# Performance work log

Measured on AMD Instinct MI355X. Metric: run time of the kernel, lower is better.

## Reference

```python
import jax, jax.numpy as jnp
import numpy as np

B, LC, LQ, D = 16, 2048, 1024, 512


def setup_inputs() -> dict:
    key = jax.random.key(0)
    k1, k2, k3 = jax.random.split(key, 3)
    context = jax.random.normal(k1, (B, LC, D), dtype=jnp.float32)
    query = jax.random.normal(k2, (LQ, D), dtype=jnp.float32)
    # nn.Linear(3*D, 1, bias=False).weight  -> [1, 3D]
    w = jax.random.normal(k3, (1, 3 * D), dtype=jnp.float32) * (1.0 / np.sqrt(3 * D))
    return {"context": context, "query": query, "w": w}


def reference(context, query, w):
    # context: [B, Lc, D], query: [Lq, D], w: [1, 3D]
    d = context.shape[-1]
    wc, wq, wm = w[0, :d], w[0, d:2 * d], w[0, 2 * d:]
    # S[b,i,j] = <context[b,i], wc> + <query[j], wq> + <context[b,i]*wm, query[j]>
    # (algebraic collapse of Linear(cat(c, q, c*q)) -- identical math, no 4D tensor)
    S = ((context @ wc)[:, :, None]
         + (query @ wq)[None, None, :]
         + jnp.einsum('bid,jd->bij', context * wm, query))  # [B, Lc, Lq]
    # softmax over context dim (dim=1), then permute -> A[b,j,i]
    A = jnp.transpose(jax.nn.softmax(S, axis=1), (0, 2, 1))  # [B, Lq, Lc]
    # query mask: sign(|sum_d query|), same for every batch element
    qmask = jnp.sign(jnp.abs(jnp.sum(query, axis=-1)))  # [Lq]
    A = A * qmask[None, :, None]
    # attd[b,j,i,d] = A[b,j,i] * context[b,i,d]
    # G_att[b,i,d] = context[b,i,d] * sum_j A[b,j,i]
    colsum = jnp.sum(A, axis=1)  # [B, Lc]
    G_att = context * colsum[:, :, None]  # [B, Lc, D]
    # H[b,j,d] = sum_i A[b,j,i] * context[b,i,d]
    H = jnp.einsum('bji,bid->bjd', A, context)  # [B, Lq, D]
    G = jnp.concatenate((context, G_att), axis=2)  # [B, Lc, 2D]
    return (G, H)
```

## Files before the change

### kernel.cpp

```cpp
#include <hip/hip_runtime.h>
#include <stdint.h>

#define BB 16
#define LC 2048
#define LQ 1024
#define DD 512

typedef _Float16 f16x8 __attribute__((ext_vector_type(8)));
typedef _Float16 f16x4 __attribute__((ext_vector_type(4)));
typedef float f32x4 __attribute__((ext_vector_type(4)));

#define MFMA16 __builtin_amdgcn_mfma_f32_16x16x32_f16

__global__ void zero_k(float* __restrict__ p, int n) {
    int i = blockIdx.x * blockDim.x + threadIdx.x;
    if (i < n) p[i] = 0.0f;
}

__global__ __launch_bounds__(256) void prep_ctx(
    const float* __restrict__ ctx, const float* __restrict__ w,
    _Float16* __restrict__ cm, _Float16* __restrict__ ct, float* __restrict__ cb)
{
    __shared__ _Float16 sm[64][68];
    const int b = blockIdx.z;
    const int i0 = blockIdx.y * 64;
    const int d0 = blockIdx.x * 64;
    const int t = threadIdx.x;
    const int tx = t & 15, ty = t >> 4;
    const float* wc = w;
    const float* wm = w + 2 * DD;
    const float4 wc4 = *(const float4*)(wc + d0 + tx * 4);
    const float4 wm4 = *(const float4*)(wm + d0 + tx * 4);
    for (int k = 0; k < 4; ++k) {
        const int r = ty + 16 * k;
        const int ig = i0 + r;
        const float4 v = *(const float4*)(ctx + ((size_t)(b * LC + ig)) * DD + d0 + tx * 4);
        f16x4 cmv = { (_Float16)(v.x * wm4.x), (_Float16)(v.y * wm4.y),
                      (_Float16)(v.z * wm4.z), (_Float16)(v.w * wm4.w) };
        *(f16x4*)(cm + ((size_t)(b * LC + ig)) * DD + d0 + tx * 4) = cmv;
        sm[tx * 4 + 0][r] = (_Float16)v.x;
        sm[tx * 4 + 1][r] = (_Float16)v.y;
        sm[tx * 4 + 2][r] = (_Float16)v.z;
        sm[tx * 4 + 3][r] = (_Float16)v.w;
        float p = v.x * wc4.x + v.y * wc4.y + v.z * wc4.z + v.w * wc4.w;
        p += __shfl_xor(p, 1); p += __shfl_xor(p, 2);
        p += __shfl_xor(p, 4); p += __shfl_xor(p, 8);
        if (tx == 0) atomicAdd(&cb[b * LC + ig], p);
    }
    __syncthreads();
    for (int k = 0; k < 4; ++k) {
        const int dd = ty + 16 * k;
        f16x4 o = *(const f16x4*)(&sm[dd][tx * 4]);
        *(f16x4*)(ct + ((size_t)(b * DD + d0 + dd)) * LC + i0 + tx * 4) = o;
    }
}

__global__ __launch_bounds__(128) void prep_q(
    const float* __restrict__ q, const float* __restrict__ w,
    _Float16* __restrict__ qh, float* __restrict__ qb, float* __restrict__ qmask)
{
    const int j = blockIdx.x;
    const int t = threadIdx.x;
    const float* wq = w + DD;
    const float4 v = *(const float4*)(q + (size_t)j * DD + t * 4);
    const float4 wq4 = *(const float4*)(wq + t * 4);
    f16x4 qv = { (_Float16)v.x, (_Float16)v.y, (_Float16)v.z, (_Float16)v.w };
    *(f16x4*)(qh + (size_t)j * DD + t * 4) = qv;
    float dq = v.x * wq4.x + v.y * wq4.y + v.z * wq4.z + v.w * wq4.w;
    float sq = v.x + v.y + v.z + v.w;
    for (int m = 1; m < 64; m <<= 1) { dq += __shfl_xor(dq, m); sq += __shfl_xor(sq, m); }
    __shared__ float sd[2], ss[2];
    if ((t & 63) == 0) { sd[t >> 6] = dq; ss[t >> 6] = sq; }
    __syncthreads();
    if (t == 0) {
        qb[j] = sd[0] + sd[1];
        float s = ss[0] + ss[1];
        qmask[j] = (s != 0.0f) ? 1.0f : 0.0f;
    }
}

__global__ __launch_bounds__(256) void gemm1(
    const _Float16* __restrict__ qh, const _Float16* __restrict__ cm,
    const float* __restrict__ cb, const float* __restrict__ qb,
    _Float16* __restrict__ E, float* __restrict__ lsum)
{
    __shared__ __align__(16) _Float16 smA[128 * 40];
    __shared__ __align__(16) _Float16 smB[128 * 40];
    const int b = blockIdx.z;
    const int m0 = blockIdx.x * 128;
    const int n0 = blockIdx.y * 128;
    const int t = threadIdx.x;
    const int lane = t & 63;
    const int wid = t >> 6;
    const int wvm = wid >> 1, wvn = wid & 1;
    const int li = lane & 15, lg = lane >> 4;
    f32x4 acc[4][4] = {};
    const int sr = t >> 1;
    const int sc = (t & 1) * 16;
    const _Float16* Ap = qh + (size_t)(m0 + sr) * DD + sc;
    const _Float16* Bp = cm + ((size_t)(b * LC + n0 + sr)) * DD + sc;
    _Float16* sAp = smA + sr * 40 + sc;
    _Float16* sBp = smB + sr * 40 + sc;
    for (int ks = 0; ks < DD; ks += 32) {
        uint4 a0 = *(const uint4*)(Ap + ks);
        uint4 a1 = *(const uint4*)(Ap + ks + 8);
        uint4 b0 = *(const uint4*)(Bp + ks);
        uint4 b1 = *(const uint4*)(Bp + ks + 8);
        __syncthreads();
        *(uint4*)(sAp) = a0;
        *(uint4*)(sAp + 8) = a1;
        *(uint4*)(sBp) = b0;
        *(uint4*)(sBp + 8) = b1;
        __syncthreads();
        const int ch = lg * 8;
        f16x8 af[4], bf[4];
        #pragma unroll
        for (int mt = 0; mt < 4; ++mt)
            af[mt] = *(const f16x8*)(smA + (wvm * 64 + mt * 16 + li) * 40 + ch);
        #pragma unroll
        for (int nt = 0; nt < 4; ++nt)
            bf[nt] = *(const f16x8*)(smB + (wvn * 64 + nt * 16 + li) * 40 + ch);
        #pragma unroll
        for (int mt = 0; mt < 4; ++mt)
            #pragma unroll
            for (int nt = 0; nt < 4; ++nt)
                acc[mt][nt] = MFMA16(af[mt], bf[nt], acc[mt][nt], 0, 0, 0);
    }
    __syncthreads();
    float* rs = (float*)smA;
    if (t < 128) rs[t] = 0.0f;
    __syncthreads();
    float cbv[4];
    #pragma unroll
    for (int nt = 0; nt < 4; ++nt) cbv[nt] = cb[b * LC + n0 + wvn * 64 + nt * 16 + li];
    #pragma unroll
    for (int mt = 0; mt < 4; ++mt) {
        #pragma unroll
        for (int r = 0; r < 4; ++r) {
            const int jl = wvm * 64 + mt * 16 + lg * 4 + r;
            const int j = m0 + jl;
            const float qbv = qb[j];
            _Float16* Erow = E + ((size_t)(b * LQ + j)) * LC + n0 + wvn * 64;
            float rsv = 0.0f;
            #pragma unroll
            for (int nt = 0; nt < 4; ++nt) {
                float e = __expf(acc[mt][nt][r] + cbv[nt] + qbv);
                rsv += e;
                Erow[nt * 16 + li] = (_Float16)e;
            }
            rsv += __shfl_xor(rsv, 1); rsv += __shfl_xor(rsv, 2);
            rsv += __shfl_xor(rsv, 4); rsv += __shfl_xor(rsv, 8);
            if (li == 0) atomicAdd(&rs[jl], rsv);
        }
    }
    __syncthreads();
    if (t < 128) atomicAdd(&lsum[b * LQ + m0 + t], rs[t]);
}

__global__ __launch_bounds__(256) void gemm2(
    const _Float16* __restrict__ E, const _Float16* __restrict__ ct,
    const float* __restrict__ lsum, const float* __restrict__ qmask,
    float* __restrict__ H)
{
    __shared__ __align__(16) _Float16 smA[128 * 40];
    __shared__ __align__(16) _Float16 smB[128 * 40];
    const int b = blockIdx.z;
    const int m0 = blockIdx.x * 128;
    const int n0 = blockIdx.y * 128;
    const int t = threadIdx.x;
    const int lane = t & 63;
    const int wid = t >> 6;
    const int wvm = wid >> 1, wvn = wid & 1;
    const int li = lane & 15, lg = lane >> 4;
    f32x4 acc[4][4] = {};
    const int sr = t >> 1;
    const int sc = (t & 1) * 16;
    const _Float16* Ap = E + ((size_t)(b * LQ + m0 + sr)) * LC + sc;
    const _Float16* Bp = ct + ((size_t)(b * DD + n0 + sr)) * LC + sc;
    _Float16* sAp = smA + sr * 40 + sc;
    _Float16* sBp = smB + sr * 40 + sc;
    for (int ks = 0; ks < LC; ks += 32) {
        uint4 a0 = *(const uint4*)(Ap + ks);
        uint4 a1 = *(const uint4*)(Ap + ks + 8);
        uint4 b0 = *(const uint4*)(Bp + ks);
        uint4 b1 = *(const uint4*)(Bp + ks + 8);
        __syncthreads();
        *(uint4*)(sAp) = a0;
        *(uint4*)(sAp + 8) = a1;
        *(uint4*)(sBp) = b0;
        *(uint4*)(sBp + 8) = b1;
        __syncthreads();
        const int ch = lg * 8;
        f16x8 af[4], bf[4];
        #pragma unroll
        for (int mt = 0; mt < 4; ++mt)
            af[mt] = *(const f16x8*)(smA + (wvm * 64 + mt * 16 + li) * 40 + ch);
        #pragma unroll
        for (int nt = 0; nt < 4; ++nt)
            bf[nt] = *(const f16x8*)(smB + (wvn * 64 + nt * 16 + li) * 40 + ch);
        #pragma unroll
        for (int mt = 0; mt < 4; ++mt)
            #pragma unroll
            for (int nt = 0; nt < 4; ++nt)
                acc[mt][nt] = MFMA16(af[mt], bf[nt], acc[mt][nt], 0, 0, 0);
    }
    #pragma unroll
    for (int mt = 0; mt < 4; ++mt) {
        #pragma unroll
        for (int r = 0; r < 4; ++r) {
            const int j = m0 + wvm * 64 + mt * 16 + lg * 4 + r;
            const float s = qmask[j] / lsum[b * LQ + j];
            float* Hrow = H + ((size_t)(b * LQ + j)) * DD + n0 + wvn * 64;
            #pragma unroll
            for (int nt = 0; nt < 4; ++nt)
                Hrow[nt * 16 + li] = acc[mt][nt][r] * s;
        }
    }
}

__global__ __launch_bounds__(256) void colsum_k(
    const _Float16* __restrict__ E, const float* __restrict__ lsum,
    const float* __restrict__ qmask, float* __restrict__ cs)
{
    __shared__ float ssm[256];
    const int b = blockIdx.z;
    const int i = blockIdx.x * 256 + threadIdx.x;
    const int j0 = blockIdx.y * 256;
    const int jj = j0 + threadIdx.x;
    ssm[threadIdx.x] = qmask[jj] / lsum[b * LQ + jj];
    __syncthreads();
    const _Float16* Eb = E + ((size_t)(b * LQ + j0)) * LC + i;
    float acc = 0.0f;
    #pragma unroll 4
    for (int j = 0; j < 256; ++j)
        acc += (float)Eb[(size_t)j * LC] * ssm[j];
    atomicAdd(&cs[b * LC + i], acc);
}

__global__ __launch_bounds__(128) void gwrite(
    const float* __restrict__ ctx, const float* __restrict__ cs, float* __restrict__ G)
{
    const int b = blockIdx.y, i = blockIdx.x, t = threadIdx.x;
    const float c = cs[b * LC + i];
    const size_t ro = (size_t)(b * LC + i);
    const float4 v = *(const float4*)(ctx + ro * DD + t * 4);
    float4 u; u.x = v.x * c; u.y = v.y * c; u.z = v.z * c; u.w = v.w * c;
    *(float4*)(G + ro * (2 * DD) + t * 4) = v;
    *(float4*)(G + ro * (2 * DD) + DD + t * 4) = u;
}

extern "C" void kernel_launch(void* const* d_in, const int* in_sizes, int n_in,
                              void* d_out, int out_size, void* d_ws, size_t ws_size,
                              hipStream_t stream)
{
    (void)in_sizes; (void)n_in; (void)out_size; (void)ws_size;
    const float* ctx = (const float*)d_in[0];
    const float* qry = (const float*)d_in[1];
    const float* w   = (const float*)d_in[2];
    float* G = (float*)d_out;
    float* H = G + (size_t)BB * LC * (2 * DD);

    char* ws = (char*)d_ws;
    _Float16* E  = (_Float16*)ws;
    _Float16* cm = (_Float16*)(ws + ((size_t)64 << 20));
    _Float16* ct = (_Float16*)(ws + ((size_t)96 << 20));
    _Float16* qh = (_Float16*)(ws + ((size_t)128 << 20));
    float* stats = (float*)(ws + ((size_t)130 << 20));
    float* cb    = stats;
    float* lsum  = cb + BB * LC;
    float* cs    = lsum + BB * LQ;
    float* qb    = cs + BB * LC;
    float* qmask = qb + LQ;

    const int nzero = BB * LC + BB * LQ + BB * LC;
    zero_k<<<dim3((nzero + 255) / 256), 256, 0, stream>>>(stats, nzero);
    prep_ctx<<<dim3(DD / 64, LC / 64, BB), 256, 0, stream>>>(ctx, w, cm, ct, cb);
    prep_q<<<dim3(LQ), 128, 0, stream>>>(qry, w, qh, qb, qmask);
    gemm1<<<dim3(LQ / 128, LC / 128, BB), 256, 0, stream>>>(qh, cm, cb, qb, E, lsum);
    gemm2<<<dim3(LQ / 128, DD / 128, BB), 256, 0, stream>>>(E, ct, lsum, qmask, H);
    colsum_k<<<dim3(LC / 256, LQ / 256, BB), 256, 0, stream>>>(E, lsum, qmask, cs);
    gwrite<<<dim3(LC, BB), 128, 0, stream>>>(ctx, cs, G);
}
```

Baseline: 404.5 us.

## Use direct global-to-LDS async loads in GEMMs and vectorize colsum kernel

Both GEMM kernels now stage tiles with global_load_lds (16-byte direct-to-LDS loads) instead of going through registers, and drop the padded LDS stride from 40 to 32. The aim is to cut register-staging instructions and VGPR pressure. Without padding, the fragment reads may hit LDS bank conflicts. The colsum kernel is also restructured so each thread reads 8 contiguous halves per row over 64 rows, giving wider loads, and then does 8 atomics per thread.

```diff
diff --git a/kernel.cpp b/kernel.cpp
--- a/kernel.cpp
+++ b/kernel.cpp
@@ -11,6 +11,12 @@
 typedef float f32x4 __attribute__((ext_vector_type(4)));
 
 #define MFMA16 __builtin_amdgcn_mfma_f32_16x16x32_f16
+
+__device__ __forceinline__ void async16(_Float16* lds, const _Float16* g) {
+    __builtin_amdgcn_global_load_lds(
+        (const __attribute__((address_space(1))) void*)g,
+        (__attribute__((address_space(3))) void*)lds, 16, 0, 0);
+}
 
 __global__ void zero_k(float* __restrict__ p, int n) {
     int i = blockIdx.x * blockDim.x + threadIdx.x;
@@ -84,8 +90,8 @@
     const float* __restrict__ cb, const float* __restrict__ qb,
     _Float16* __restrict__ E, float* __restrict__ lsum)
 {
-    __shared__ __align__(16) _Float16 smA[128 * 40];
-    __shared__ __align__(16) _Float16 smB[128 * 40];
+    __shared__ __align__(16) _Float16 smA[128 * 32];
+    __shared__ __align__(16) _Float16 smB[128 * 32];
     const int b = blockIdx.z;
     const int m0 = blockIdx.x * 128;
     const int n0 = blockIdx.y * 128;
@@ -95,31 +101,30 @@
     const int wvm = wid >> 1, wvn = wid & 1;
     const int li = lane & 15, lg = lane >> 4;
     f32x4 acc[4][4] = {};
-    const int sr = t >> 1;
-    const int sc = (t & 1) * 16;
-    const _Float16* Ap = qh + (size_t)(m0 + sr) * DD + sc;
-    const _Float16* Bp = cm + ((size_t)(b * LC + n0 + sr)) * DD + sc;
-    _Float16* sAp = smA + sr * 40 + sc;
-    _Float16* sBp = smB + sr * 40 + sc;
+    const int srow = lane >> 2;
+    const int scol = (lane & 3) * 8;
+    const _Float16* gA0 = qh + (size_t)(m0 + wid * 32 + srow) * DD + scol;
+    const _Float16* gA1 = gA0 + (size_t)16 * DD;
+    const _Float16* gB0 = cm + ((size_t)(b * LC + n0 + wid * 32 + srow)) * DD + scol;
+    const _Float16* gB1 = gB0 + (size_t)16 * DD;
+    _Float16* sA0 = smA + wid * 32 * 32;
+    _Float16* sA1 = sA0 + 16 * 32;
+    _Float16* sB0 = smB + wid * 32 * 32;
+    _Float16* sB1 = sB0 + 16 * 32;
     for (int ks = 0; ks < DD; ks += 32) {
-        uint4 a0 = *(const uint4*)(Ap + ks);
-        uint4 a1 = *(const uint4*)(Ap + ks + 8);
-        uint4 b0 = *(const uint4*)(Bp + ks);
-        uint4 b1 = *(const uint4*)(Bp + ks + 8);
-        __syncthreads();
-        *(uint4*)(sAp) = a0;
-        *(uint4*)(sAp + 8) = a1;
-        *(uint4*)(sBp) = b0;
-        *(uint4*)(sBp + 8) = b1;
-        __syncthreads();
-        const int ch = lg * 8;
+        __syncthreads();
+        async16(sA0, gA0 + ks);
+        async16(sA1, gA1 + ks);
+        async16(sB0, gB0 + ks);
+        async16(sB1, gB1 + ks);
+        __syncthreads();
         f16x8 af[4], bf[4];
         #pragma unroll
         for (int mt = 0; mt < 4; ++mt)
-            af[mt] = *(const f16x8*)(smA + (wvm * 64 + mt * 16 + li) * 40 + ch);
+            af[mt] = *(const f16x8*)(smA + (wvm * 64 + mt * 16 + li) * 32 + lg * 8);
         #pragma unroll
         for (int nt = 0; nt < 4; ++nt)
-            bf[nt] = *(const f16x8*)(smB + (wvn * 64 + nt * 16 + li) * 40 + ch);
+            bf[nt] = *(const f16x8*)(smB + (wvn * 64 + nt * 16 + li) * 32 + lg * 8);
         #pragma unroll
         for (int mt = 0; mt < 4; ++mt)
             #pragma unroll
@@ -162,8 +167,8 @@
     const float* __restrict__ lsum, const float* __restrict__ qmask,
     float* __restrict__ H)
 {
-    __shared__ __align__(16) _Float16 smA[128 * 40];
-    __shared__ __align__(16) _Float16 smB[128 * 40];
+    __shared__ __align__(16) _Float16 smA[128 * 32];
+    __shared__ __align__(16) _Float16 smB[128 * 32];
     const int b = blockIdx.z;
     const int m0 = blockIdx.x * 128;
     const int n0 = blockIdx.y * 128;
@@ -173,31 +178,30 @@
     const int wvm = wid >> 1, wvn = wid & 1;
     const int li = lane & 15, lg = lane >> 4;
     f32x4 acc[4][4] = {};
-    const int sr = t >> 1;
-    const int sc = (t & 1) * 16;
-    const _Float16* Ap = E + ((size_t)(b * LQ + m0 + sr)) * LC + sc;
-    const _Float16* Bp = ct + ((size_t)(b * DD + n0 + sr)) * LC + sc;
-    _Float16* sAp = smA + sr * 40 + sc;
-    _Float16* sBp = smB + sr * 40 + sc;
+    const int srow = lane >> 2;
+    const int scol = (lane & 3) * 8;
+    const _Float16* gA0 = E + ((size_t)(b * LQ + m0 + wid * 32 + srow)) * LC + scol;
+    const _Float16* gA1 = gA0 + (size_t)16 * LC;
+    const _Float16* gB0 = ct + ((size_t)(b * DD + n0 + wid * 32 + srow)) * LC + scol;
+    const _Float16* gB1 = gB0 + (size_t)16 * LC;
+    _Float16* sA0 = smA + wid * 32 * 32;
+    _Float16* sA1 = sA0 + 16 * 32;
+    _Float16* sB0 = smB + wid * 32 * 32;
+    _Float16* sB1 = sB0 + 16 * 32;
     for (int ks = 0; ks < LC; ks += 32) {
-        uint4 a0 = *(const uint4*)(Ap + ks);
-        uint4 a1 = *(const uint4*)(Ap + ks + 8);
-        uint4 b0 = *(const uint4*)(Bp + ks);
-        uint4 b1 = *(const uint4*)(Bp + ks + 8);
-        __syncthreads();
-        *(uint4*)(sAp) = a0;
-        *(uint4*)(sAp + 8) = a1;
-        *(uint4*)(sBp) = b0;
-        *(uint4*)(sBp + 8) = b1;
-        __syncthreads();
-        const int ch = lg * 8;
+        __syncthreads();
+        async16(sA0, gA0 + ks);
+        async16(sA1, gA1 + ks);
+        async16(sB0, gB0 + ks);
+        async16(sB1, gB1 + ks);
+        __syncthreads();
         f16x8 af[4], bf[4];
         #pragma unroll
         for (int mt = 0; mt < 4; ++mt)
-            af[mt] = *(const f16x8*)(smA + (wvm * 64 + mt * 16 + li) * 40 + ch);
+            af[mt] = *(const f16x8*)(smA + (wvm * 64 + mt * 16 + li) * 32 + lg * 8);
         #pragma unroll
         for (int nt = 0; nt < 4; ++nt)
-            bf[nt] = *(const f16x8*)(smB + (wvn * 64 + nt * 16 + li) * 40 + ch);
+            bf[nt] = *(const f16x8*)(smB + (wvn * 64 + nt * 16 + li) * 32 + lg * 8);
         #pragma unroll
         for (int mt = 0; mt < 4; ++mt)
             #pragma unroll
@@ -222,19 +226,27 @@
     const _Float16* __restrict__ E, const float* __restrict__ lsum,
     const float* __restrict__ qmask, float* __restrict__ cs)
 {
-    __shared__ float ssm[256];
-    const int b = blockIdx.z;
-    const int i = blockIdx.x * 256 + threadIdx.x;
-    const int j0 = blockIdx.y * 256;
-    const int jj = j0 + threadIdx.x;
-    ssm[threadIdx.x] = qmask[jj] / lsum[b * LQ + jj];
-    __syncthreads();
-    const _Float16* Eb = E + ((size_t)(b * LQ + j0)) * LC + i;
-    float acc = 0.0f;
+    __shared__ float ssm[64];
+    const int b = blockIdx.y;
+    const int j0 = blockIdx.x * 64;
+    const int t = threadIdx.x;
+    if (t < 64) {
+        const int jj = j0 + t;
+        ssm[t] = qmask[jj] / lsum[b * LQ + jj];
+    }
+    __syncthreads();
+    const _Float16* Eb = E + ((size_t)(b * LQ + j0)) * LC + t * 8;
+    float acc[8] = {};
     #pragma unroll 4
-    for (int j = 0; j < 256; ++j)
-        acc += (float)Eb[(size_t)j * LC] * ssm[j];
-    atomicAdd(&cs[b * LC + i], acc);
+    for (int j = 0; j < 64; ++j) {
+        f16x8 v = *(const f16x8*)(Eb + (size_t)j * LC);
+        const float s = ssm[j];
+        #pragma unroll
+        for (int q = 0; q < 8; ++q) acc[q] += s * (float)v[q];
+    }
+    float* base = cs + b * LC + t * 8;
+    #pragma unroll
+    for (int q = 0; q < 8; ++q) atomicAdd(base + q, acc[q]);
 }
 
 __global__ __launch_bounds__(128) void gwrite(
@@ -278,6 +290,6 @@
     prep_q<<<dim3(LQ), 128, 0, stream>>>(qry, w, qh, qb, qmask);
     gemm1<<<dim3(LQ / 128, LC / 128, BB), 256, 0, stream>>>(qh, cm, cb, qb, E, lsum);
     gemm2<<<dim3(LQ / 128, DD / 128, BB), 256, 0, stream>>>(E, ct, lsum, qmask, H);
-    colsum_k<<<dim3(LC / 256, LQ / 256, BB), 256, 0, stream>>>(E, lsum, qmask, cs);
+    colsum_k<<<dim3(LQ / 64, BB), 256, 0, stream>>>(E, lsum, qmask, cs);
     gwrite<<<dim3(LC, BB), 128, 0, stream>>>(ctx, cs, G);
 }
```

Result: faster. 391.5 us (-3.2%).
